# Kernel tuning notes

Measured on AMD Instinct MI355X. Metric: run time of the kernel, lower is better.

Reference implementation:

```python
import jax, jax.numpy as jnp
import numpy as np


def setup_inputs() -> dict:
    key = jax.random.key(0)
    k1, k2, k3 = jax.random.split(key, 3)
    B, T, F = 32, 8192, 80
    ODIM, IDIM = 1024, 640
    src_tokens = jax.random.normal(k1, (B, T, F), dtype=jnp.float32)
    src_lengths = jax.random.randint(k2, (B,), 3, T + 1, dtype=jnp.int64)
    # xavier_normal_ on Linear weight [odim, idim]
    std = float(np.sqrt(2.0 / (ODIM + IDIM)))
    W = jax.random.normal(k3, (ODIM, IDIM), dtype=jnp.float32) * std
    b = jnp.zeros((ODIM,), dtype=jnp.float32)
    return {"src_tokens": src_tokens, "src_lengths": src_lengths, "W": W, "b": b}


def reference(src_tokens, src_lengths, W, b):
    B, T, F = src_tokens.shape
    n_frames = (T // 3) * 3
    out_lengths = src_lengths // 3 - 2
    # stack 3 consecutive frames: cat(x[:, ::3], x[:, 1::3], x[:, 2::3], -1) == reshape
    x = src_tokens[:, :n_frames, :].reshape(B, n_frames // 3, 3 * F)  # [B, M, 240]
    # window of 3 stacked frames -> feature 9F = 720, then keep first 640
    x = jnp.concatenate((x[:, :-2, :], x[:, 1:-1, :], x[:, 2:, :]), axis=-1)  # [B, M-2, 720]
    x = x[:, :, : x.shape[-1] - 80]  # [B, M-2, 640]
    x = jnp.transpose(x, (1, 0, 2))  # [T', B, 640]
    y = jnp.einsum("tbi,oi->tbo", x, W) + b  # [T', B, odim]
    # GLU on dim=1 (the batch dim, as in the original code)
    half = y.shape[1] // 2
    x_out = y[:, :half, :] * jax.nn.sigmoid(y[:, half:, :])  # [T', B/2, odim]
    return (x_out, out_lengths)
```

## Files before the change

### kernel.cpp

```cpp
#include <hip/hip_runtime.h>

#define GLOBAL_AS __attribute__((address_space(1)))
#define LDS_AS    __attribute__((address_space(3)))

typedef __bf16 bf16x8 __attribute__((ext_vector_type(8)));
typedef float  f32x4  __attribute__((ext_vector_type(4)));

constexpr int SRC_STRIDE = 8192 * 80;
constexpr int TOUT       = 2728;
constexpr long OUT_ELEMS = (long)TOUT * 16 * 1024;
constexpr int SRC_ELEMS  = 32 * SRC_STRIDE;
constexpr int W_ELEMS    = 1024 * 640;
constexpr int MBLK       = 682;

__device__ __forceinline__ unsigned short f2bf(float f) {
    union { float f; unsigned u; } a; a.f = f;
    unsigned r = a.u + 0x7FFF + ((a.u >> 16) & 1);
    return (unsigned short)(r >> 16);
}

__global__ void cvt_kernel(const float* __restrict__ in, unsigned short* __restrict__ out, int n4) {
    int i = blockIdx.x * blockDim.x + threadIdx.x;
    if (i >= n4) return;
    float4 v = ((const float4*)in)[i];
    ushort4 o;
    o.x = f2bf(v.x); o.y = f2bf(v.y); o.z = f2bf(v.z); o.w = f2bf(v.w);
    ((ushort4*)out)[i] = o;
}

__global__ void lengths_kernel(const int* __restrict__ len, float* __restrict__ out) {
    int i = threadIdx.x;
    if (i < 32) out[OUT_ELEMS + i] = (float)(len[i] / 3 - 2);
}

__global__ void glu_gemm(const __bf16* __restrict__ A,
                         const __bf16* __restrict__ Wb,
                         const float* __restrict__ bias,
                         float* __restrict__ out) {
    __shared__ __bf16 lA[128 * 64];
    __shared__ __bf16 lB[128 * 64];

    const int tid  = threadIdx.x;
    const int lane = tid & 63;
    const int w    = tid >> 6;
    const int wm   = w & 1;
    const int wn   = w >> 1;

    const int bid = blockIdx.x;
    const int bn  = (bid >> 3) & 7;
    const int bm  = (bid >> 6) * 8 + (bid & 7);
    if (bm >= MBLK) return;

    const int c8 = (((lane & 7) ^ (lane >> 3)) * 8);
    int aoff_g[4], boff_g[4];
#pragma unroll
    for (int j = 0; j < 4; ++j) {
        int r = w * 32 + j * 8 + (lane >> 3);
        int m = bm * 128 + r;
        int t = m >> 5, b = m & 31;
        aoff_g[j] = b * SRC_STRIDE + t * 240 + c8;
        int n = bn * 128 + r;
        boff_g[j] = n * 640 + c8;
    }

    const int q    = lane >> 4;
    const int poff = ((q ^ (lane & 7)) * 8);
    int aoff_l[4], boff_l[4];
#pragma unroll
    for (int i = 0; i < 4; ++i) {
        aoff_l[i] = (wm * 64 + i * 16 + (lane & 15)) * 64;
        boff_l[i] = (wn * 64 + i * 16 + (lane & 15)) * 64;
    }

    f32x4 acc[4][4] = {};

    for (int kb = 0; kb < 10; ++kb) {
        const int k0 = kb * 64;
#pragma unroll
        for (int j = 0; j < 4; ++j) {
            __builtin_amdgcn_global_load_lds(
                (const GLOBAL_AS void*)(A + (aoff_g[j] + k0)),
                (LDS_AS void*)(lA + (w * 32 + j * 8) * 64), 16, 0, 0);
            __builtin_amdgcn_global_load_lds(
                (const GLOBAL_AS void*)(Wb + (boff_g[j] + k0)),
                (LDS_AS void*)(lB + (w * 32 + j * 8) * 64), 16, 0, 0);
        }
        __syncthreads();
#pragma unroll
        for (int ks = 0; ks < 2; ++ks) {
            const int po = poff ^ (ks << 5);
            bf16x8 af[4], bfv[4];
#pragma unroll
            for (int i = 0; i < 4; ++i)
                af[i] = *(const bf16x8*)(lA + aoff_l[i] + po);
#pragma unroll
            for (int i = 0; i < 4; ++i)
                bfv[i] = *(const bf16x8*)(lB + boff_l[i] + po);
#pragma unroll
            for (int mt = 0; mt < 4; ++mt)
#pragma unroll
                for (int nt = 0; nt < 4; ++nt)
                    acc[mt][nt] = __builtin_amdgcn_mfma_f32_16x16x32_bf16(
                        af[mt], bfv[nt], acc[mt][nt], 0, 0, 0);
        }
        __syncthreads();
    }

    const int col = lane & 15;
    float bv[4];
#pragma unroll
    for (int nt = 0; nt < 4; ++nt)
        bv[nt] = bias[bn * 128 + wn * 64 + nt * 16 + col];

    const int t_base = bm * 4 + wm * 2;
#pragma unroll
    for (int pr = 0; pr < 2; ++pr) {
        const int t = t_base + pr;
#pragma unroll
        for (int nt = 0; nt < 4; ++nt) {
            const int n = bn * 128 + wn * 64 + nt * 16 + col;
#pragma unroll
            for (int r2 = 0; r2 < 4; ++r2) {
                const int brow = q * 4 + r2;
                float v = acc[pr * 2 + 0][nt][r2] + bv[nt];
                float g = acc[pr * 2 + 1][nt][r2] + bv[nt];
                float s = 1.0f / (1.0f + __expf(-g));
                out[((long)(t * 16 + brow)) * 1024 + n] = v * s;
            }
        }
    }
}

extern "C" void kernel_launch(void* const* d_in, const int* in_sizes, int n_in,
                              void* d_out, int out_size, void* d_ws, size_t ws_size,
                              hipStream_t stream) {
    const float* src  = (const float*)d_in[0];
    const int*   lens = (const int*)d_in[1];
    const float* Wf   = (const float*)d_in[2];
    const float* bias = (const float*)d_in[3];
    float* out = (float*)d_out;

    unsigned short* srcb = (unsigned short*)d_ws;
    unsigned short* wb   = srcb + SRC_ELEMS;

    cvt_kernel<<<SRC_ELEMS / 4 / 256, 256, 0, stream>>>(src, srcb, SRC_ELEMS / 4);
    cvt_kernel<<<W_ELEMS / 4 / 256, 256, 0, stream>>>(Wf, wb, W_ELEMS / 4);

    lengths_kernel<<<1, 64, 0, stream>>>(lens, out);

    glu_gemm<<<86 * 64, 256, 0, stream>>>((const __bf16*)srcb, (const __bf16*)wb, bias, out);
}
```

Before: 349.2 us.

## Keep full-K weight slice resident in LDS, stream A from registers with 32x32 MFMA

Replaces the double-LDS tiled GEMM with a kernel that loads a block's entire 64-column weight slice (all K) into LDS once, pre-arranged into MFMA fragment order by a new weight conversion kernel. A operands are read directly from global memory into registers with software prefetch, and each wave computes one time step across all 32 batch rows using 32x32x16 MFMAs, so the GLU pairs fall within a single accumulator. The intent is to drop the per-k-step syncthreads and A-tile LDS traffic. In exchange, A reloads are no longer shared through LDS, each block uses 80KB of LDS which limits occupancy, and A global loads sit directly on the critical path.

```diff
diff --git a/kernel.cpp b/kernel.cpp
--- a/kernel.cpp
+++ b/kernel.cpp
@@ -4,14 +4,14 @@
 #define LDS_AS    __attribute__((address_space(3)))
 
 typedef __bf16 bf16x8 __attribute__((ext_vector_type(8)));
-typedef float  f32x4  __attribute__((ext_vector_type(4)));
+typedef float  f32x16 __attribute__((ext_vector_type(16)));
 
 constexpr int SRC_STRIDE = 8192 * 80;
 constexpr int TOUT       = 2728;
 constexpr long OUT_ELEMS = (long)TOUT * 16 * 1024;
 constexpr int SRC_ELEMS  = 32 * SRC_STRIDE;
 constexpr int W_ELEMS    = 1024 * 640;
-constexpr int MBLK       = 682;
+constexpr int MBLK       = 341;
 
 __device__ __forceinline__ unsigned short f2bf(float f) {
     union { float f; unsigned u; } a; a.f = f;
@@ -28,105 +28,112 @@
     ((ushort4*)out)[i] = o;
 }
 
+__global__ void cvt_w_frag(const float* __restrict__ W, unsigned short* __restrict__ out) {
+    int i = blockIdx.x * blockDim.x + threadIdx.x;
+    int nl = i & 63;
+    int c  = (i >> 6) % 80;
+    int bn = i / 5120;
+    const float* src = W + (bn * 64 + nl) * 640 + c * 8;
+    float4 v0 = ((const float4*)src)[0];
+    float4 v1 = ((const float4*)src)[1];
+    ushort4 o0, o1;
+    o0.x = f2bf(v0.x); o0.y = f2bf(v0.y); o0.z = f2bf(v0.z); o0.w = f2bf(v0.w);
+    o1.x = f2bf(v1.x); o1.y = f2bf(v1.y); o1.z = f2bf(v1.z); o1.w = f2bf(v1.w);
+    ((ushort4*)(out + (long)i * 8))[0] = o0;
+    ((ushort4*)(out + (long)i * 8))[1] = o1;
+}
+
 __global__ void lengths_kernel(const int* __restrict__ len, float* __restrict__ out) {
     int i = threadIdx.x;
     if (i < 32) out[OUT_ELEMS + i] = (float)(len[i] / 3 - 2);
 }
 
-__global__ void glu_gemm(const __bf16* __restrict__ A,
-                         const __bf16* __restrict__ Wb,
-                         const float* __restrict__ bias,
-                         float* __restrict__ out) {
-    __shared__ __bf16 lA[128 * 64];
-    __shared__ __bf16 lB[128 * 64];
+__global__ __launch_bounds__(512, 4) void glu_gemm(
+        const __bf16* __restrict__ A,
+        const __bf16* __restrict__ Wfrag,
+        const float* __restrict__ bias,
+        float* __restrict__ out) {
+    __shared__ __bf16 lB[40960];
 
     const int tid  = threadIdx.x;
     const int lane = tid & 63;
     const int w    = tid >> 6;
-    const int wm   = w & 1;
-    const int wn   = w >> 1;
+    const int b    = lane & 31;
+    const int q    = lane >> 5;
 
     const int bid = blockIdx.x;
-    const int bn  = (bid >> 3) & 7;
-    const int bm  = (bid >> 6) * 8 + (bid & 7);
+    const int bn  = (bid >> 3) & 15;
+    const int bm  = (bid >> 7) * 8 + (bid & 7);
     if (bm >= MBLK) return;
 
-    const int c8 = (((lane & 7) ^ (lane >> 3)) * 8);
-    int aoff_g[4], boff_g[4];
+    const __bf16* wsrc = Wfrag + (long)bn * 40960;
 #pragma unroll
-    for (int j = 0; j < 4; ++j) {
-        int r = w * 32 + j * 8 + (lane >> 3);
-        int m = bm * 128 + r;
-        int t = m >> 5, b = m & 31;
-        aoff_g[j] = b * SRC_STRIDE + t * 240 + c8;
-        int n = bn * 128 + r;
-        boff_g[j] = n * 640 + c8;
+    for (int i = 0; i < 10; ++i) {
+        __builtin_amdgcn_global_load_lds(
+            (const GLOBAL_AS void*)(wsrc + i * 4096 + tid * 8),
+            (LDS_AS void*)(lB + i * 4096 + tid * 8), 16, 0, 0);
     }
 
-    const int q    = lane >> 4;
-    const int poff = ((q ^ (lane & 7)) * 8);
-    int aoff_l[4], boff_l[4];
+    const int t_w = bm * 8 + w;
+    const __bf16* aptr = A + ((long)b * SRC_STRIDE + t_w * 240 + q * 8);
+
+    const int bbase = q * 512 + b * 8;
+
+    bf16x8 aC[2], aN[2], bC[2][2], bN[2][2];
+    aC[0] = *(const bf16x8*)(aptr);
+    aC[1] = *(const bf16x8*)(aptr + 16);
+
+    __syncthreads();
+
+    bC[0][0] = *(const bf16x8*)(lB + bbase);
+    bC[0][1] = *(const bf16x8*)(lB + bbase + 1024);
+    bC[1][0] = *(const bf16x8*)(lB + bbase + 256);
+    bC[1][1] = *(const bf16x8*)(lB + bbase + 1024 + 256);
+
+    f32x16 acc[2] = {};
+
 #pragma unroll
-    for (int i = 0; i < 4; ++i) {
-        aoff_l[i] = (wm * 64 + i * 16 + (lane & 15)) * 64;
-        boff_l[i] = (wn * 64 + i * 16 + (lane & 15)) * 64;
+    for (int kc = 0; kc < 20; ++kc) {
+        if (kc < 19) {
+            const int k2 = (kc + 1) * 32;
+            aN[0] = *(const bf16x8*)(aptr + k2);
+            aN[1] = *(const bf16x8*)(aptr + k2 + 16);
+            const int lb = (kc + 1) * 2048 + bbase;
+            bN[0][0] = *(const bf16x8*)(lB + lb);
+            bN[0][1] = *(const bf16x8*)(lB + lb + 1024);
+            bN[1][0] = *(const bf16x8*)(lB + lb + 256);
+            bN[1][1] = *(const bf16x8*)(lB + lb + 1024 + 256);
+        }
+#pragma unroll
+        for (int s = 0; s < 2; ++s) {
+#pragma unroll
+            for (int nt = 0; nt < 2; ++nt)
+                acc[nt] = __builtin_amdgcn_mfma_f32_32x32x16_bf16(
+                    aC[s], bC[nt][s], acc[nt], 0, 0, 0);
+        }
+#pragma unroll
+        for (int s = 0; s < 2; ++s) { aC[s] = aN[s]; }
+#pragma unroll
+        for (int nt = 0; nt < 2; ++nt) {
+            bC[nt][0] = bN[nt][0]; bC[nt][1] = bN[nt][1];
+        }
     }
 
-    f32x4 acc[4][4] = {};
+    const int n0 = bn * 64 + b;
+    float bv0 = bias[n0];
+    float bv1 = bias[n0 + 32];
 
-    for (int kb = 0; kb < 10; ++kb) {
-        const int k0 = kb * 64;
 #pragma unroll
-        for (int j = 0; j < 4; ++j) {
-            __builtin_amdgcn_global_load_lds(
-                (const GLOBAL_AS void*)(A + (aoff_g[j] + k0)),
-                (LDS_AS void*)(lA + (w * 32 + j * 8) * 64), 16, 0, 0);
-            __builtin_amdgcn_global_load_lds(
-                (const GLOBAL_AS void*)(Wb + (boff_g[j] + k0)),
-                (LDS_AS void*)(lB + (w * 32 + j * 8) * 64), 16, 0, 0);
-        }
-        __syncthreads();
+    for (int nt = 0; nt < 2; ++nt) {
+        const float bvv = nt ? bv1 : bv0;
+        const long ncol = n0 + nt * 32;
 #pragma unroll
-        for (int ks = 0; ks < 2; ++ks) {
-            const int po = poff ^ (ks << 5);
-            bf16x8 af[4], bfv[4];
-#pragma unroll
-            for (int i = 0; i < 4; ++i)
-                af[i] = *(const bf16x8*)(lA + aoff_l[i] + po);
-#pragma unroll
-            for (int i = 0; i < 4; ++i)
-                bfv[i] = *(const bf16x8*)(lB + boff_l[i] + po);
-#pragma unroll
-            for (int mt = 0; mt < 4; ++mt)
-#pragma unroll
-                for (int nt = 0; nt < 4; ++nt)
-                    acc[mt][nt] = __builtin_amdgcn_mfma_f32_16x16x32_bf16(
-                        af[mt], bfv[nt], acc[mt][nt], 0, 0, 0);
-        }
-        __syncthreads();
-    }
-
-    const int col = lane & 15;
-    float bv[4];
-#pragma unroll
-    for (int nt = 0; nt < 4; ++nt)
-        bv[nt] = bias[bn * 128 + wn * 64 + nt * 16 + col];
-
-    const int t_base = bm * 4 + wm * 2;
-#pragma unroll
-    for (int pr = 0; pr < 2; ++pr) {
-        const int t = t_base + pr;
-#pragma unroll
-        for (int nt = 0; nt < 4; ++nt) {
-            const int n = bn * 128 + wn * 64 + nt * 16 + col;
-#pragma unroll
-            for (int r2 = 0; r2 < 4; ++r2) {
-                const int brow = q * 4 + r2;
-                float v = acc[pr * 2 + 0][nt][r2] + bv[nt];
-                float g = acc[pr * 2 + 1][nt][r2] + bv[nt];
-                float s = 1.0f / (1.0f + __expf(-g));
-                out[((long)(t * 16 + brow)) * 1024 + n] = v * s;
-            }
+        for (int r = 0; r < 8; ++r) {
+            const int brow = (r & 3) + 8 * (r >> 2) + 4 * q;
+            float v = acc[nt][r] + bvv;
+            float g = acc[nt][r + 8] + bvv;
+            float s = 1.0f / (1.0f + __expf(-g));
+            out[((long)(t_w * 16 + brow)) * 1024 + ncol] = v * s;
         }
     }
 }
@@ -140,13 +147,14 @@
     const float* bias = (const float*)d_in[3];
     float* out = (float*)d_out;
 
-    unsigned short* srcb = (unsigned short*)d_ws;
-    unsigned short* wb   = srcb + SRC_ELEMS;
+    unsigned short* srcb  = (unsigned short*)d_ws;
+    unsigned short* wfrag = srcb + SRC_ELEMS;
 
     cvt_kernel<<<SRC_ELEMS / 4 / 256, 256, 0, stream>>>(src, srcb, SRC_ELEMS / 4);
-    cvt_kernel<<<W_ELEMS / 4 / 256, 256, 0, stream>>>(Wf, wb, W_ELEMS / 4);
+    cvt_w_frag<<<W_ELEMS / 8 / 256, 256, 0, stream>>>(Wf, wfrag);
 
     lengths_kernel<<<1, 64, 0, stream>>>(lens, out);
 
-    glu_gemm<<<86 * 64, 256, 0, stream>>>((const __bf16*)srcb, (const __bf16*)wb, bias, out);
+    glu_gemm<<<43 * 128, 512, 0, stream>>>((const __bf16*)srcb,
+                                           (const __bf16*)wfrag, bias, out);
 }
```

Result: slower. 443.7 us (+27.0%).
